# Optimization experiments

Measured on AMD Instinct MI355X. Metric: run time of the kernel, lower is better.

The kernel has to match this reference:

```python
import jax, jax.numpy as jnp
import numpy as np

B, N, NPOINT = 8, 2048, 1024
K = 32
C_IN, C_OUT = 128, 256
PLANES = C_IN // 2   # bottleneck_ratio = 2
MID = PLANES // 2
CURVE_NUM, CURVE_LEN = 100, 5
RADIUS = 0.2
EPS = 1e-5


def bn(x, g, b):
    # training-mode batchnorm over all axes except channel axis 1
    axes = tuple(i for i in range(x.ndim) if i != 1)
    m = jnp.mean(x, axes, keepdims=True)
    v = jnp.var(x, axes, keepdims=True)
    shp = [1] * x.ndim
    shp[1] = -1
    return (x - m) * jax.lax.rsqrt(v + EPS) * g.reshape(shp) + b.reshape(shp)


def conv1d(w, x):  # 1x1 conv, w [O,I], x [B,I,n]
    return jnp.einsum('oi,bin->bon', w, x)


def conv2d(w, x):  # 1x1 conv, w [O,I], x [B,I,n,k]
    return jnp.einsum('oi,bink->bonk', w, x)


def lrelu(x):
    return jax.nn.leaky_relu(x, 0.2)


def gather_points(pts, idx):
    # pts [B,n,C], idx [B,...] int -> [B,...,C]
    b = pts.shape[0]
    out = jnp.take_along_axis(pts, idx.reshape(b, -1)[:, :, None], axis=1)
    return out.reshape(idx.shape + (pts.shape[-1],))


def fps(xyz, npoint):
    # deterministic FPS (torch code zeroes the random start -> index 0)
    bsz, n, _ = xyz.shape
    bidx = jnp.arange(bsz)

    def body(carry, _):
        dist, far = carry
        c = xyz[bidx, far]  # [B,3]
        d = jnp.sum((xyz - c[:, None, :]) ** 2, axis=-1)
        dist = jnp.minimum(dist, d)
        return (dist, jnp.argmax(dist, axis=-1).astype(jnp.int32)), far

    init = (jnp.full((bsz, n), 1e10, xyz.dtype), jnp.zeros((bsz,), jnp.int32))
    _, cents = jax.lax.scan(body, init, None, length=npoint)
    return jnp.transpose(cents)  # [B,npoint]


def knn_idx(pts, k):
    # pts [B,3,n] -> [B,n,k+1] nearest neighbors (self included)
    inner = jnp.einsum('bcn,bcm->bnm', pts, pts)
    xx = jnp.sum(pts * pts, axis=1)
    neg = 2.0 * inner - xx[:, :, None] - xx[:, None, :]
    return jax.lax.top_k(neg, k + 1)[1]


def ball_query(radius, nsample, xyz, new_xyz):
    n = xyz.shape[1]
    sqr = (jnp.sum(new_xyz ** 2, -1)[:, :, None] + jnp.sum(xyz ** 2, -1)[:, None, :]
           - 2.0 * jnp.einsum('bsc,bnc->bsn', new_xyz, xyz))
    gidx = jnp.where(sqr > radius ** 2, n,
                     jnp.arange(n, dtype=jnp.int32)[None, None, :])
    gidx = jnp.sort(gidx, axis=-1)[:, :, :nsample]
    return jnp.where(gidx == n, gidx[:, :, :1], gidx)


def st_gumbel_softmax(logits):
    # straight-through softmax (no gumbel noise, T=1), one-hot over last dim
    y = jax.nn.softmax(logits, axis=-1)
    hard = jax.nn.one_hot(jnp.argmax(y, axis=-1), y.shape[-1], dtype=y.dtype)
    return y + jax.lax.stop_gradient(hard - y)


def walk(x, adj, start, aw, ag, ab, mw, mg, mb):
    # x [B,c,n] attended feats, adj [B,n,K] neighbor idx, start [B,cn]
    xt = jnp.transpose(x, (0, 2, 1))  # [B,n,c]
    cur = start
    pre = jnp.transpose(gather_points(xt, cur), (0, 2, 1))[..., None]  # [B,c,cn,1]
    cur_f = cur_cos = pre_cos = None
    curves = []
    for step in range(CURVE_LEN):
        if step > 0:
            cat = jnp.concatenate([cur_f[..., 0], pre[..., 0]], axis=1)  # [B,2c,cn]
            att = jax.nn.softmax(bn(conv1d(mw, cat), mg, mb), axis=1)    # [B,2,cn]
            att = jnp.transpose(att, (0, 2, 1))[:, None]                 # [B,1,cn,2]
            pre = jnp.sum(jnp.concatenate([cur_f, pre], axis=-1) * att,
                          axis=-1, keepdims=True)
            pre_cos = jnp.transpose(pre[..., 0], (0, 2, 1))              # [B,cn,c]
        pick_idx = jnp.take_along_axis(adj, cur[:, :, None], axis=1)     # [B,cn,K]
        pv = gather_points(xt, pick_idx)                                 # [B,cn,K,c]
        pvt = jnp.transpose(pv, (0, 3, 1, 2))                            # [B,c,cn,K]
        agent_in = jnp.concatenate([pvt, jnp.broadcast_to(pre, pvt.shape)], axis=1)
        logits = bn(conv2d(aw, agent_in), ag, ab)                        # [B,1,cn,K]
        if step > 0:
            a = jax.lax.stop_gradient(cur_cos - pre_cos)                 # [B,cn,c]
            nb = jax.lax.stop_gradient(pv - cur_cos[:, :, None, :])      # [B,cn,K,c]
            dot = jnp.einsum('bnc,bnkc->bnk', a, nb)
            den = jnp.maximum(jnp.linalg.norm(a, axis=-1)[:, :, None]
                              * jnp.linalg.norm(nb, axis=-1), 1e-8)
            d = jnp.clip(1.0 + dot / den, 0.0, 1.0)
            logits = logits * d[:, None]
        w = st_gumbel_softmax(logits)                                    # [B,1,cn,K]
        cur_f = jnp.sum(pvt * w, axis=-1, keepdims=True)                 # [B,c,cn,1]
        cur_cos = jnp.transpose(cur_f[..., 0], (0, 2, 1))
        cur = jnp.argmax(w[:, 0], axis=-1).astype(jnp.int32)
        curves.append(cur_f)
    return jnp.concatenate(curves, axis=-1)  # [B,c,cn,CL]


def curve_agg(x, curves, la, wa, wb, wc, wn, wl, wd, dg, db):
    att = conv2d(la, curves)                                             # [B,1,cn,cl]
    inter = jnp.sum(curves * jax.nn.softmax(att, axis=-1), axis=-1)      # [B,c,cn]
    intra = jnp.sum(curves * jax.nn.softmax(att, axis=-2), axis=-2)      # [B,c,cl]
    inter = conv1d(wa, inter)
    intra = conv1d(wb, intra)
    xl = jnp.transpose(conv1d(wc, x), (0, 2, 1))                         # [B,n,mid]
    x_inter = jax.nn.softmax(jnp.einsum('bnm,bmk->bnk', xl, inter), axis=-1)
    x_intra = jax.nn.softmax(jnp.einsum('bnm,bml->bnl', xl, intra), axis=-1)
    inter_n = jnp.transpose(conv1d(wn, inter), (0, 2, 1))                # [B,cn,mid]
    intra_l = jnp.transpose(conv1d(wl, intra), (0, 2, 1))                # [B,cl,mid]
    cf = jnp.concatenate([jnp.einsum('bnk,bkm->bnm', x_inter, inter_n),
                          jnp.einsum('bnl,blm->bnm', x_intra, intra_l)], axis=-1)
    return lrelu(x + bn(conv1d(wd, jnp.transpose(cf, (0, 2, 1))), dg, db))


def lpfa(x, xyz, idx, xw, xg, xb, w1, g1, b1, w2, g2, b2):
    # x [B,c,n], xyz [B,n,3], idx [B,n,K]
    nb_xyz = gather_points(xyz, idx)                                     # [B,n,K,3]
    pts = xyz[:, :, None, :]
    pf = jnp.concatenate([jnp.broadcast_to(pts, nb_xyz.shape), nb_xyz, nb_xyz - pts],
                         axis=-1)                                        # [B,n,K,9]
    pf = jnp.transpose(pf, (0, 3, 1, 2))                                 # [B,9,n,K]
    xt = jnp.transpose(x, (0, 2, 1))
    f = gather_points(xt, idx) - xt[:, :, None, :]                       # [B,n,K,c]
    f = jnp.transpose(f, (0, 3, 1, 2))                                   # [B,c,n,K]
    f = lrelu(f + bn(conv2d(xw, pf), xg, xb))
    f = lrelu(bn(conv2d(w1, f), g1, b1))
    f = lrelu(bn(conv2d(w2, f), g2, b2))
    return jnp.mean(f, axis=-1)                                          # [B,c,n]


def cic_forward(xyz, x, conv1_w, conv1_g, conv1_b, conv2_w, conv2_g, conv2_b,
                sc_w, sc_g, sc_b, cg_att_w, wk_agent_w, wk_agent_g, wk_agent_b,
                wk_mom_w, wk_mom_g, wk_mom_b, ca_la_w, ca_a_w, ca_b_w, ca_c_w,
                ca_n_w, ca_l_w, ca_d_w, ca_d_g, ca_d_b, lp_x2f_w, lp_x2f_g,
                lp_x2f_b, lp_m1_w, lp_m1_g, lp_m1_b, lp_m2_w, lp_m2_g, lp_m2_b):
    xyz_t = jnp.transpose(xyz, (0, 2, 1))                                # [B,N,3]
    # MaskedMaxPool: FPS -> ball query -> grouped max
    new_xyz = gather_points(xyz_t, fps(xyz_t, NPOINT))                   # [B,np,3]
    gidx = ball_query(RADIUS, K, xyz_t, new_xyz)                         # [B,np,K]
    grouped = gather_points(jnp.transpose(x, (0, 2, 1)), gidx)           # [B,np,K,C]
    x = jnp.transpose(jnp.max(grouped, axis=2), (0, 2, 1))               # [B,C_IN,np]
    xyz_d = jnp.transpose(new_xyz, (0, 2, 1))                            # [B,3,np]
    shortcut = x
    h = lrelu(bn(conv1d(conv1_w, x), conv1_g, conv1_b))                  # [B,P,np]
    idx = knn_idx(xyz_d, K)                                              # [B,np,K+1]
    # CurveGrouping: attention-weighted start point selection + walk
    x_att = jax.nn.sigmoid(conv1d(cg_att_w, h))                          # [B,1,np]
    start = jax.lax.top_k(x_att[:, 0, :], CURVE_NUM)[1].astype(jnp.int32)
    curves = walk(h * x_att, idx[:, :, 1:], start,
                  wk_agent_w, wk_agent_g, wk_agent_b,
                  wk_mom_w, wk_mom_g, wk_mom_b)
    h = curve_agg(h, curves, ca_la_w, ca_a_w, ca_b_w, ca_c_w, ca_n_w, ca_l_w,
                  ca_d_w, ca_d_g, ca_d_b)
    h = lpfa(h, new_xyz, idx[:, :, :K], lp_x2f_w, lp_x2f_g, lp_x2f_b,
             lp_m1_w, lp_m1_g, lp_m1_b, lp_m2_w, lp_m2_g, lp_m2_b)
    out = bn(conv1d(conv2_w, h), conv2_g, conv2_b)
    sc = bn(conv1d(sc_w, shortcut), sc_g, sc_b)
    return xyz_d, lrelu(out + sc)


def setup_inputs() -> dict:
    key = jax.random.key(0)
    ks = iter(jax.random.split(key, 64))

    def w(shape):
        return jax.random.normal(next(ks), shape, jnp.float32) / np.float32(np.sqrt(shape[-1]))

    P, M = PLANES, MID
    return dict(
        xyz=jax.random.uniform(next(ks), (B, 3, N), jnp.float32),
        x=jax.random.normal(next(ks), (B, C_IN, N), jnp.float32),
        conv1_w=w((P, C_IN)), conv1_g=jnp.ones(P), conv1_b=jnp.zeros(P),
        conv2_w=w((C_OUT, P)), conv2_g=jnp.ones(C_OUT), conv2_b=jnp.zeros(C_OUT),
        sc_w=w((C_OUT, C_IN)), sc_g=jnp.ones(C_OUT), sc_b=jnp.zeros(C_OUT),
        cg_att_w=w((1, P)),
        wk_agent_w=w((1, 2 * P)), wk_agent_g=jnp.ones(1), wk_agent_b=jnp.zeros(1),
        wk_mom_w=w((2, 2 * P)), wk_mom_g=jnp.ones(2), wk_mom_b=jnp.zeros(2),
        ca_la_w=w((1, P)),
        ca_a_w=w((M, P)), ca_b_w=w((M, P)), ca_c_w=w((M, P)),
        ca_n_w=w((M, M)), ca_l_w=w((M, M)),
        ca_d_w=w((P, 2 * M)), ca_d_g=jnp.ones(P), ca_d_b=jnp.zeros(P),
        lp_x2f_w=w((P, 9)), lp_x2f_g=jnp.ones(P), lp_x2f_b=jnp.zeros(P),
        lp_m1_w=w((P, P)), lp_m1_g=jnp.ones(P), lp_m1_b=jnp.zeros(P),
        lp_m2_w=w((P, P)), lp_m2_g=jnp.ones(P), lp_m2_b=jnp.zeros(P),
    )


def reference(xyz, x, conv1_w, conv1_g, conv1_b, conv2_w, conv2_g, conv2_b,
              sc_w, sc_g, sc_b, cg_att_w, wk_agent_w, wk_agent_g, wk_agent_b,
              wk_mom_w, wk_mom_g, wk_mom_b, ca_la_w, ca_a_w, ca_b_w, ca_c_w,
              ca_n_w, ca_l_w, ca_d_w, ca_d_g, ca_d_b, lp_x2f_w, lp_x2f_g,
              lp_x2f_b, lp_m1_w, lp_m1_g, lp_m1_b, lp_m2_w, lp_m2_g, lp_m2_b):
    return cic_forward(xyz, x, conv1_w, conv1_g, conv1_b, conv2_w, conv2_g,
                       conv2_b, sc_w, sc_g, sc_b, cg_att_w, wk_agent_w,
                       wk_agent_g, wk_agent_b, wk_mom_w, wk_mom_g, wk_mom_b,
                       ca_la_w, ca_a_w, ca_b_w, ca_c_w, ca_n_w, ca_l_w, ca_d_w,
                       ca_d_g, ca_d_b, lp_x2f_w, lp_x2f_g, lp_x2f_b, lp_m1_w,
                       lp_m1_g, lp_m1_b, lp_m2_w, lp_m2_g, lp_m2_b)
```

## Files before the change

kernel.cpp:

```cpp
#include <hip/hip_runtime.h>
#include <math.h>

namespace {

constexpr int BB = 8;
constexpr int NN = 2048;
constexpr int NP = 1024;
constexpr int KS = 32;
constexpr int CI = 128;
constexpr int CO = 256;
constexpr int PL = 64;
constexpr int MD = 32;
constexpr int CN = 100;
constexpr int CLn = 5;
constexpr float R2v = 0.04f;
constexpr float EPSF = 1e-5f;

#define DEV static __device__ __forceinline__

DEV float lrelu(float x){ return x >= 0.0f ? x : 0.2f * x; }

DEV float wsum64(float v){
#pragma unroll
  for (int m = 32; m; m >>= 1) v += __shfl_xor(v, m, 64);
  return v;
}

DEV unsigned long long dpp_wavemax_u64(unsigned long long v){
  unsigned hi = (unsigned)(v >> 32), lo = (unsigned)v;
#define DSTEP(ctrl) { \
    unsigned nhi = (unsigned)__builtin_amdgcn_update_dpp((int)hi, (int)hi, ctrl, 0xf, 0xf, false); \
    unsigned nlo = (unsigned)__builtin_amdgcn_update_dpp((int)lo, (int)lo, ctrl, 0xf, 0xf, false); \
    bool gt = (nhi > hi) || (nhi == hi && nlo > lo); \
    hi = gt ? nhi : hi; lo = gt ? nlo : lo; }
  DSTEP(0x111)
  DSTEP(0x112)
  DSTEP(0x114)
  DSTEP(0x118)
  DSTEP(0x142)
  DSTEP(0x143)
#undef DSTEP
  hi = (unsigned)__builtin_amdgcn_readlane((int)hi, 63);
  lo = (unsigned)__builtin_amdgcn_readlane((int)lo, 63);
  return ((unsigned long long)hi << 32) | lo;
}

DEV int dpp_argmax_idx(float v, int idx){
  unsigned kb = __float_as_uint(v);
  kb = (kb & 0x80000000u) ? ~kb : (kb | 0x80000000u);
  unsigned long long p = ((unsigned long long)kb << 32) | (unsigned)~idx;
  return (int)~(unsigned)dpp_wavemax_u64(p);
}

__global__ __launch_bounds__(256) void k_fps(const float* __restrict__ xyz,
                                             float* __restrict__ nxyz, float* __restrict__ nxx){
  int b = blockIdx.x, t = threadIdx.x, w = t >> 6;
  const float* X = xyz + (size_t)b*3*NN;
  __shared__ unsigned long long sk[2][4];
  __shared__ float4 scd[2][4];
  float px[8], py[8], pz[8], dd[8];
  int base = t*8;
#pragma unroll
  for (int j=0;j<8;++j){
    px[j]=X[base+j]; py[j]=X[NN+base+j]; pz[j]=X[2*NN+base+j];
    dd[j]=1e10f;
  }
  float cx = X[0], cy = X[NN], cz = X[2*NN];
  float ox[4], oy[4], oz[4];
#pragma unroll
  for (int p=0;p<4;++p){
    for (int j=0;j<256;++j){
      if (j == t){ ox[p]=cx; oy[p]=cy; oz[p]=cz; }
#pragma unroll
      for (int q=0;q<8;++q){
        float dx=__fsub_rn(px[q],cx), dy=__fsub_rn(py[q],cy), dz=__fsub_rn(pz[q],cz);
        float dn=__fadd_rn(__fadd_rn(__fmul_rn(dx,dx),__fmul_rn(dy,dy)),__fmul_rn(dz,dz));
        dd[q] = fminf(dd[q], dn);
      }
      float v = dd[0]; int li = 0;
#pragma unroll
      for (int q=1;q<8;++q) if (dd[q] > v){ v = dd[q]; li = q; }
      float wx = px[0], wy = py[0], wz = pz[0];
#pragma unroll
      for (int q=1;q<8;++q) if (li == q){ wx=px[q]; wy=py[q]; wz=pz[q]; }
      unsigned long long key = ((unsigned long long)__float_as_uint(v) << 32) | (unsigned)~(base+li);
      unsigned long long wm = dpp_wavemax_u64(key);
      if (key == wm){ sk[j&1][w] = wm; scd[j&1][w] = make_float4(wx,wy,wz,0.f); }
      __syncthreads();
      unsigned long long k0=sk[j&1][0], k1=sk[j&1][1], k2=sk[j&1][2], k3=sk[j&1][3];
      float4 c0=scd[j&1][0], c1=scd[j&1][1], c2=scd[j&1][2], c3=scd[j&1][3];
      if (k1 > k0){ k0=k1; c0=c1; }
      if (k2 > k0){ k0=k2; c0=c2; }
      if (k3 > k0){ k0=k3; c0=c3; }
      cx = c0.x; cy = c0.y; cz = c0.z;
    }
  }
#pragma unroll
  for (int p=0;p<4;++p){
    size_t o = (size_t)(b*NP + (p<<8) + t);
    nxyz[o*3+0]=ox[p]; nxyz[o*3+1]=oy[p]; nxyz[o*3+2]=oz[p];
    nxx[o] = __fadd_rn(__fadd_rn(__fmul_rn(ox[p],ox[p]),__fmul_rn(oy[p],oy[p])),__fmul_rn(oz[p],oz[p]));
  }
}

__global__ __launch_bounds__(256) void k_ball(const float* __restrict__ xyz,
                      const float* __restrict__ nxyz, const float* __restrict__ nxx,
                      int* __restrict__ gidx){
  __shared__ int lists[4][KS];
  int t = threadIdx.x, w = t>>6, lane = t&63;
  int s = blockIdx.x*4 + w;
  int b = s >> 10;
  const float* X = xyz + (size_t)b*3*NN;
  float cx = nxyz[s*3], cy = nxyz[s*3+1], cz = nxyz[s*3+2];
  float cn = nxx[s];
  unsigned long long lmask = (lane == 63) ? 0x7fffffffffffffffull : ((1ull<<lane)-1ull);
  int cnt = 0;
  for (int ch = 0; ch < NN/64; ++ch){
    int n = ch*64 + lane;
    float px = X[n], py = X[NN+n], pz = X[2*NN+n];
    float nrm = __fadd_rn(__fadd_rn(__fmul_rn(px,px),__fmul_rn(py,py)),__fmul_rn(pz,pz));
    float dot = __fadd_rn(__fadd_rn(__fmul_rn(cx,px),__fmul_rn(cy,py)),__fmul_rn(cz,pz));
    float sqr = __fsub_rn(__fadd_rn(cn, nrm), __fmul_rn(2.0f, dot));
    bool inr = !(sqr > R2v);
    unsigned long long m = __ballot(inr);
    if (inr){
      int slot = cnt + __popcll(m & lmask);
      if (slot < KS) lists[w][slot] = n;
    }
    cnt += __popcll(m);
    if (cnt >= KS) break;
  }
  int take = cnt < KS ? cnt : KS;
  if (lane < KS){
    gidx[(size_t)s*KS + lane] = lists[w][lane < take ? lane : 0];
  }
}

__global__ __launch_bounds__(256) void k_transpose(const float* __restrict__ x, float* __restrict__ xt){
  __shared__ float tile[32][33];
  int blk = blockIdx.x;
  int b = blk >> 8;
  int r = blk & 255;
  int nt = r >> 2, ct = r & 3;
  int tx = threadIdx.x & 31, ty = threadIdx.x >> 5;
  const float* Xb = x + (size_t)b*CI*NN;
#pragma unroll
  for (int q=0;q<4;++q){
    int row = ty + q*8;
    tile[row][tx] = Xb[(size_t)(ct*32+row)*NN + nt*32 + tx];
  }
  __syncthreads();
  float* Tb = xt + (size_t)b*NN*CI;
#pragma unroll
  for (int q=0;q<4;++q){
    int row = ty + q*8;
    Tb[(size_t)(nt*32+row)*CI + ct*32 + tx] = tile[tx][row];
  }
}

__global__ __launch_bounds__(128) void k_groupmax(const float* __restrict__ xt, const int* __restrict__ gidx,
                          float* __restrict__ xnew){
  int s = blockIdx.x;
  int b = s >> 10;
  int c = threadIdx.x;
  const int* gi = gidx + (size_t)s*KS;
  float m = -INFINITY;
#pragma unroll 4
  for (int k=0;k<KS;++k){
    int idx = gi[k];
    m = fmaxf(m, xt[((size_t)b*NN + idx)*CI + c]);
  }
  xnew[(size_t)s*CI + c] = m;
}

__global__ __launch_bounds__(256) void k_conv1(const float* __restrict__ xnew, const float* __restrict__ w,
                       float* __restrict__ hraw, float* __restrict__ part){
  __shared__ float wl[PL*129];
  __shared__ float xr[4][CI];
  __shared__ float ssm[4][PL], sq[4][PL];
  int t = threadIdx.x, wid = t>>6, lane = t&63;
  for (int u=t; u<PL*CI; u+=256){ int c=u>>7, i=u&127; wl[c*129+i] = w[u]; }
  int pt = blockIdx.x*4 + wid;
  xr[wid][lane]      = xnew[(size_t)pt*CI + lane];
  xr[wid][lane+64]   = xnew[(size_t)pt*CI + lane + 64];
  __syncthreads();
  float acc = 0.f;
  for (int i=0;i<CI;++i) acc = __fadd_rn(acc, __fmul_rn(wl[lane*129+i], xr[wid][i]));
  hraw[(size_t)pt*PL + lane] = acc;
  ssm[wid][lane] = acc; sq[wid][lane] = acc*acc;
  __syncthreads();
  if (t < PL){
    float s=0,q=0;
#pragma unroll
    for (int k=0;k<4;++k){ s+=ssm[k][t]; q+=sq[k][t]; }
    part[((size_t)blockIdx.x*PL + t)*2]   = s;
    part[((size_t)blockIdx.x*PL + t)*2+1] = q;
  }
}

__global__ __launch_bounds__(256) void k_red(const float* __restrict__ part, float* __restrict__ mv,
                     int nblk, int C2){
  int slot = blockIdx.x;
  __shared__ float red[256];
  float s = 0;
  for (int i = threadIdx.x; i < nblk; i += 256) s += part[(size_t)i*C2 + slot];
  red[threadIdx.x] = s; __syncthreads();
  for (int off=128; off; off>>=1){ if (threadIdx.x < off) red[threadIdx.x] += red[threadIdx.x+off]; __syncthreads(); }
  if (threadIdx.x==0) mv[slot] = red[0];
}

__global__ __launch_bounds__(256) void k_n1(const float* __restrict__ hraw, const float* __restrict__ mv,
                    const float* __restrict__ g, const float* __restrict__ bb_, const float* __restrict__ attw,
                    float* __restrict__ h, float* __restrict__ attv, float* __restrict__ wxt){
  int t=threadIdx.x, wid=t>>6, lane=t&63;
  int pt = blockIdx.x*4 + wid;
  float x = hraw[(size_t)pt*PL + lane];
  float m = mv[2*lane] * (1.0f/8192.0f);
  float var = fmaxf(mv[2*lane+1]*(1.0f/8192.0f) - m*m, 0.f);
  float rs = 1.0f/sqrtf(var + EPSF);
  float hv = lrelu(__fadd_rn(__fmul_rn(__fmul_rn(__fsub_rn(x,m),rs), g[lane]), bb_[lane]));
  h[(size_t)pt*PL + lane] = hv;
  float dotv = wsum64(__fmul_rn(hv, attw[lane]));
  float att = 1.0f/(1.0f + expf(-dotv));
  if (lane==0) attv[pt] = att;
  wxt[(size_t)pt*PL + lane] = __fmul_rn(hv, att);
}

__global__ __launch_bounds__(256) void k_knn(const float* __restrict__ nxyz, const float* __restrict__ nxx,
                     int* __restrict__ knnI){
  int t=threadIdx.x, wid=t>>6, lane=t&63;
  int gn = blockIdx.x*4 + wid;
  int b = gn >> 10;
  float cx = nxyz[(size_t)gn*3], cy=nxyz[(size_t)gn*3+1], cz=nxyz[(size_t)gn*3+2];
  float xn = nxx[gn];
  float vals[16];
#pragma unroll
  for (int q=0;q<16;++q){
    int mm = b*NP + q*64 + lane;
    float px=nxyz[(size_t)mm*3], py=nxyz[(size_t)mm*3+1], pz=nxyz[(size_t)mm*3+2];
    float dot = __fadd_rn(__fadd_rn(__fmul_rn(cx,px),__fmul_rn(cy,py)),__fmul_rn(cz,pz));
    vals[q] = __fsub_rn(__fsub_rn(__fmul_rn(2.0f,dot), xn), nxx[mm]);
  }
  int* out = knnI + (size_t)gn*33;
  for (int j=0;j<33;++j){
    float bv = -INFINITY; int bq = 0;
#pragma unroll
    for (int q=0;q<16;++q) if (vals[q] > bv){ bv = vals[q]; bq = q; }
    int vi = dpp_argmax_idx(bv, (bq<<6) | lane);
    if (lane == 0) out[j] = vi;
    if ((vi & 63) == lane){
      int wq = vi>>6;
#pragma unroll
      for (int q=0;q<16;++q) if (q==wq) vals[q] = -INFINITY;
    }
  }
}

__global__ __launch_bounds__(64) void k_start(const float* __restrict__ attv, int* __restrict__ startb){
  int b = blockIdx.x, lane = threadIdx.x;
  float vals[16];
#pragma unroll
  for (int q=0;q<16;++q) vals[q] = attv[b*NP + q*64 + lane];
  for (int j=0;j<CN;++j){
    float bv=-INFINITY; int bq=0;
#pragma unroll
    for (int q=0;q<16;++q) if (vals[q] > bv){ bv=vals[q]; bq=q; }
    int vi = dpp_argmax_idx(bv, (bq<<6) | lane);
    if (lane==0) startb[b*CN + j] = vi;
    if ((vi&63)==lane){
      int wq=vi>>6;
#pragma unroll
      for(int q=0;q<16;++q) if(q==wq) vals[q]=-INFINITY;
    }
  }
}

__global__ __launch_bounds__(256) void k_w0(const float* __restrict__ wxt, const int* __restrict__ startb,
                    float* __restrict__ pre, int* __restrict__ curidx){
  int t=threadIdx.x, wid=t>>6, lane=t&63;
  int gc = blockIdx.x*4+wid;
  int b = gc/CN;
  int si = startb[gc];
  pre[(size_t)gc*PL + lane] = wxt[((size_t)b*NP+si)*PL + lane];
  if (lane==0) curidx[gc] = si;
}

__global__ __launch_bounds__(256) void k_wmom(const float* __restrict__ curf, float* __restrict__ pre,
                      const float* __restrict__ mw, const float* __restrict__ mg, const float* __restrict__ mb_){
  __shared__ float m0a[BB*CN], m1a[BB*CN];
  __shared__ float red[256][4];
  __shared__ float bc[4];
  int t = threadIdx.x;
  float s0=0,q0=0,s1=0,q1=0;
  for (int u=t; u<BB*CN; u+=256){
    const float4* cf4 = reinterpret_cast<const float4*>(curf + (size_t)u*PL);
    const float4* pr4 = reinterpret_cast<const float4*>(pre + (size_t)u*PL);
    float a0=0, a1=0;
#pragma unroll
    for (int i4=0;i4<16;++i4){
      float4 c = cf4[i4];
      a0=__fadd_rn(a0,__fmul_rn(mw[i4*4+0],c.x));     a0=__fadd_rn(a0,__fmul_rn(mw[i4*4+1],c.y));
      a0=__fadd_rn(a0,__fmul_rn(mw[i4*4+2],c.z));     a0=__fadd_rn(a0,__fmul_rn(mw[i4*4+3],c.w));
      a1=__fadd_rn(a1,__fmul_rn(mw[128+i4*4+0],c.x)); a1=__fadd_rn(a1,__fmul_rn(mw[128+i4*4+1],c.y));
      a1=__fadd_rn(a1,__fmul_rn(mw[128+i4*4+2],c.z)); a1=__fadd_rn(a1,__fmul_rn(mw[128+i4*4+3],c.w));
    }
#pragma unroll
    for (int i4=0;i4<16;++i4){
      float4 p = pr4[i4];
      a0=__fadd_rn(a0,__fmul_rn(mw[64+i4*4+0],p.x));  a0=__fadd_rn(a0,__fmul_rn(mw[64+i4*4+1],p.y));
      a0=__fadd_rn(a0,__fmul_rn(mw[64+i4*4+2],p.z));  a0=__fadd_rn(a0,__fmul_rn(mw[64+i4*4+3],p.w));
      a1=__fadd_rn(a1,__fmul_rn(mw[192+i4*4+0],p.x)); a1=__fadd_rn(a1,__fmul_rn(mw[192+i4*4+1],p.y));
      a1=__fadd_rn(a1,__fmul_rn(mw[192+i4*4+2],p.z)); a1=__fadd_rn(a1,__fmul_rn(mw[192+i4*4+3],p.w));
    }
    m0a[u]=a0; m1a[u]=a1;
    s0+=a0; q0+=a0*a0; s1+=a1; q1+=a1*a1;
  }
  red[t][0]=s0; red[t][1]=q0; red[t][2]=s1; red[t][3]=q1;
  __syncthreads();
  for (int off=128; off; off>>=1){
    if (t<off){ red[t][0]+=red[t+off][0]; red[t][1]+=red[t+off][1]; red[t][2]+=red[t+off][2]; red[t][3]+=red[t+off][3]; }
    __syncthreads();
  }
  if (t==0){
    float me0 = red[0][0]/800.0f, va0 = fmaxf(red[0][1]/800.0f - me0*me0, 0.f);
    float me1 = red[0][2]/800.0f, va1 = fmaxf(red[0][3]/800.0f - me1*me1, 0.f);
    bc[0]=me0; bc[1]=1.0f/sqrtf(va0+EPSF); bc[2]=me1; bc[3]=1.0f/sqrtf(va1+EPSF);
  }
  __syncthreads();
  float me0=bc[0], rs0=bc[1], me1=bc[2], rs1=bc[3];
  float g0=mg[0], g1=mg[1], b0=mb_[0], b1=mb_[1];
  for (int u=t; u<BB*CN; u+=256){
    float z0 = __fadd_rn(__fmul_rn(__fmul_rn(__fsub_rn(m0a[u],me0),rs0),g0), b0);
    float z1 = __fadd_rn(__fmul_rn(__fmul_rn(__fsub_rn(m1a[u],me1),rs1),g1), b1);
    float mx = fmaxf(z0,z1);
    float e0 = expf(z0-mx), e1 = expf(z1-mx);
    float se = e0+e1;
    float a0 = e0/se, a1 = e1/se;
    float4* pr4 = reinterpret_cast<float4*>(pre + (size_t)u*PL);
    const float4* cf4 = reinterpret_cast<const float4*>(curf + (size_t)u*PL);
#pragma unroll
    for (int c4=0;c4<16;++c4){
      float4 cv = cf4[c4], pv_ = pr4[c4], r;
      r.x = __fadd_rn(__fmul_rn(cv.x,a0), __fmul_rn(pv_.x,a1));
      r.y = __fadd_rn(__fmul_rn(cv.y,a0), __fmul_rn(pv_.y,a1));
      r.z = __fadd_rn(__fmul_rn(cv.z,a0), __fmul_rn(pv_.z,a1));
      r.w = __fadd_rn(__fmul_rn(cv.w,a0), __fmul_rn(pv_.w,a1));
      pr4[c4] = r;
    }
  }
}

__global__ __launch_bounds__(256) void k_w2(const float* __restrict__ wxt, const float* __restrict__ pre,
                    const int* __restrict__ knnI, const int* __restrict__ curidx,
                    const float* __restrict__ aw,
                    float* __restrict__ pv, float* __restrict__ logitb, float* __restrict__ part){
  __shared__ float red[256];
  __shared__ int nbrs[8][32];
  int t=threadIdx.x;
  int gcw = t>>5, k = t & 31;
  int gc0 = blockIdx.x*8;
  int gc = gc0 + gcw;
  int b = gc/CN;
  int cc = curidx[gc];
  int nbr = knnI[((size_t)b*NP + cc)*33 + 1 + k];
  nbrs[gcw][k] = nbr;
  __syncthreads();
  int lane = t & 63, w = t >> 6;
#pragma unroll 4
  for (int r = w; r < 256; r += 4){
    int rg = r >> 5, rk = r & 31;
    int rb = (gc0 + rg)/CN;
    pv[((size_t)(gc0+rg)*KS + rk)*PL + lane] = wxt[((size_t)rb*NP + nbrs[rg][rk])*PL + lane];
  }
  __syncthreads();
  const float* row = pv + ((size_t)gc*KS + k)*PL;
  const float* pr = pre + (size_t)gc*PL;
  float acc=0;
  for (int i=0;i<PL;++i){ acc=__fadd_rn(acc,__fmul_rn(aw[i],row[i])); }
  for (int i=0;i<PL;++i){ acc=__fadd_rn(acc,__fmul_rn(aw[PL+i],pr[i])); }
  logitb[(size_t)gc*KS + k] = acc;
  red[t]=acc; __syncthreads();
  for (int off=128; off; off>>=1){ if(t<off) red[t]+=red[t+off]; __syncthreads(); }
  float tot = red[0];
  __syncthreads();
  red[t]=acc*acc; __syncthreads();
  for (int off=128; off; off>>=1){ if(t<off) red[t]+=red[t+off]; __syncthreads(); }
  if (t==0){ part[blockIdx.x*2]=tot; part[blockIdx.x*2+1]=red[0]; }
}

__global__ __launch_bounds__(64) void k_w3(const float* __restrict__ pv, const float* __restrict__ logitb,
                   const float* __restrict__ part, float* __restrict__ curf,
                   const float* __restrict__ pre, float* __restrict__ curves, int* __restrict__ curidx,
                   const float* __restrict__ ag, const float* __restrict__ ab_, int step){
  __shared__ int ks_;
  __shared__ float wv_;
  int gc = blockIdx.x;
  int lane = threadIdx.x;
  float s=0,q=0;
  for (int u=lane; u<100; u+=64){ s+=part[2*u]; q+=part[2*u+1]; }
  s = wsum64(s); q = wsum64(q);
  float me = s/25600.0f;
  float va = fmaxf(q/25600.0f - me*me, 0.f);
  float rs = 1.0f/sqrtf(va+EPSF);
  float g0 = ag[0], b0 = ab_[0];
// ... 232 lines not shown
  __shared__ int   nbl[4][KS];
  __shared__ __align__(16) float fbuf[4][PL*36];
  __shared__ float ssm[4][PL], sq[4][PL];
  int t=threadIdx.x, wid=t>>6, lane=t&63;
  int pt = blockIdx.x*4+wid;
  int b = pt >> 10;
  if (lane < KS){
    int nb = knnI[(size_t)pt*33 + lane];
    nbl[wid][lane] = nb;
    float cx=nxyz[(size_t)pt*3], cy=nxyz[(size_t)pt*3+1], cz=nxyz[(size_t)pt*3+2];
    size_t nbg = (size_t)b*NP + nb;
    float nx=nxyz[nbg*3], ny=nxyz[nbg*3+1], nz=nxyz[nbg*3+2];
    float* pf = &pfb[wid][lane*10];
    pf[0]=cx; pf[1]=cy; pf[2]=cz; pf[3]=nx; pf[4]=ny; pf[5]=nz;
    pf[6]=__fsub_rn(nx,cx); pf[7]=__fsub_rn(ny,cy); pf[8]=__fsub_rn(nz,cz);
  }
  __syncthreads();
  float xwr[9];
#pragma unroll
  for (int i=0;i<9;++i) xwr[i] = xw[lane*9+i];
  float c1v[KS];
#pragma unroll
  for (int j=0;j<KS;++j){
    float a=0;
#pragma unroll
    for (int i=0;i<9;++i) a = fmaf(xwr[i], pfb[wid][j*10+i], a);
    c1v[j]=a;
  }
  if (STAGE == 1){
    float s=0,qq=0;
#pragma unroll
    for (int j=0;j<KS;++j){ s+=c1v[j]; qq+=c1v[j]*c1v[j]; }
    ssm[wid][lane]=s; sq[wid][lane]=qq;
    __syncthreads();
    if (t<PL){
      float s2=0,q2=0;
#pragma unroll
      for(int k2=0;k2<4;++k2){s2+=ssm[k2][t];q2+=sq[k2][t];}
      part[((size_t)blockIdx.x*PL+t)*2]=s2; part[((size_t)blockIdx.x*PL+t)*2+1]=q2;
    }
    return;
  }
  constexpr float CT = 1.0f/262144.0f;
  float m1 = mv1[2*lane]*CT; float va1=fmaxf(mv1[2*lane+1]*CT-m1*m1,0.f); float rs1=1.0f/sqrtf(va1+EPSF);
  float hc = h2[(size_t)pt*PL + lane];
  float g1v=g1[lane], b1v=b1[lane];
#pragma unroll
  for (int j=0;j<KS;++j){
    float fd = __fsub_rn(h2[((size_t)b*NP + nbl[wid][j])*PL + lane], hc);
    float bn1 = __fadd_rn(__fmul_rn(__fmul_rn(__fsub_rn(c1v[j],m1),rs1),g1v),b1v);
    fbuf[wid][lane*36+j] = lrelu(__fadd_rn(fd, bn1));
  }
  __syncthreads();
  float wr[PL];
#pragma unroll
  for (int i=0;i<PL;++i) wr[i] = w1[lane*PL+i];
  float acc[KS];
#pragma unroll
  for (int j=0;j<KS;++j) acc[j]=0;
#pragma unroll
  for (int cp=0;cp<PL;++cp){
    const float4* rp = reinterpret_cast<const float4*>(&fbuf[wid][cp*36]);
    float wv = wr[cp];
#pragma unroll
    for (int j4=0;j4<8;++j4){
      float4 f = rp[j4];
      acc[j4*4+0] = fmaf(wv, f.x, acc[j4*4+0]);
      acc[j4*4+1] = fmaf(wv, f.y, acc[j4*4+1]);
      acc[j4*4+2] = fmaf(wv, f.z, acc[j4*4+2]);
      acc[j4*4+3] = fmaf(wv, f.w, acc[j4*4+3]);
    }
  }
  if (STAGE == 2){
    float s=0,qq=0;
#pragma unroll
    for (int j=0;j<KS;++j){ s+=acc[j]; qq+=acc[j]*acc[j]; }
    ssm[wid][lane]=s; sq[wid][lane]=qq;
    __syncthreads();
    if (t<PL){
      float s2=0,q2=0;
#pragma unroll
      for(int k2=0;k2<4;++k2){s2+=ssm[k2][t];q2+=sq[k2][t];}
      part[((size_t)blockIdx.x*PL+t)*2]=s2; part[((size_t)blockIdx.x*PL+t)*2+1]=q2;
    }
    return;
  }
  float m2 = mv2[2*lane]*CT; float va2=fmaxf(mv2[2*lane+1]*CT-m2*m2,0.f); float rs2=1.0f/sqrtf(va2+EPSF);
  float g2v=g2[lane], b2v=b2[lane];
  __syncthreads();
#pragma unroll
  for (int j=0;j<KS;++j){
    float f2 = lrelu(__fadd_rn(__fmul_rn(__fmul_rn(__fsub_rn(acc[j],m2),rs2),g2v),b2v));
    fbuf[wid][lane*36+j] = f2;
  }
  __syncthreads();
#pragma unroll
  for (int i=0;i<PL;++i) wr[i] = w2[lane*PL+i];
#pragma unroll
  for (int j=0;j<KS;++j) acc[j]=0;
#pragma unroll
  for (int cp=0;cp<PL;++cp){
    const float4* rp = reinterpret_cast<const float4*>(&fbuf[wid][cp*36]);
    float wv = wr[cp];
#pragma unroll
    for (int j4=0;j4<8;++j4){
      float4 f = rp[j4];
      acc[j4*4+0] = fmaf(wv, f.x, acc[j4*4+0]);
      acc[j4*4+1] = fmaf(wv, f.y, acc[j4*4+1]);
      acc[j4*4+2] = fmaf(wv, f.z, acc[j4*4+2]);
      acc[j4*4+3] = fmaf(wv, f.w, acc[j4*4+3]);
    }
  }
  if (STAGE == 3){
    float s=0,qq=0;
#pragma unroll
    for (int j=0;j<KS;++j){ s+=acc[j]; qq+=acc[j]*acc[j]; }
    ssm[wid][lane]=s; sq[wid][lane]=qq;
    __syncthreads();
    if (t<PL){
      float s2=0,q2=0;
#pragma unroll
      for(int k2=0;k2<4;++k2){s2+=ssm[k2][t];q2+=sq[k2][t];}
      part[((size_t)blockIdx.x*PL+t)*2]=s2; part[((size_t)blockIdx.x*PL+t)*2+1]=q2;
    }
    return;
  }
  float m3 = mv3[2*lane]*CT; float va3=fmaxf(mv3[2*lane+1]*CT-m3*m3,0.f); float rs3=1.0f/sqrtf(va3+EPSF);
  float g3v=g3[lane], b3v=b3[lane];
  float sum=0;
#pragma unroll
  for (int j=0;j<KS;++j){
    float f3 = lrelu(__fadd_rn(__fmul_rn(__fmul_rn(__fsub_rn(acc[j],m3),rs3),g3v),b3v));
    sum = __fadd_rn(sum, f3);
  }
  lpout[(size_t)pt*PL + lane] = __fmul_rn(sum, (1.0f/32.0f));
}

__global__ __launch_bounds__(256) void k_fc1(const float* __restrict__ lpout, const float* __restrict__ w,
                     float* __restrict__ y2raw, float* __restrict__ part){
  __shared__ float wl[128*65];
  __shared__ float xr[4][PL];
  __shared__ float ssm[4][128], sq[4][128];
  int t=threadIdx.x, wid=t>>6, lane=t&63;
  int pg = blockIdx.x >> 1;
  int half = blockIdx.x & 1;
  int pt = pg*4 + wid;
  for (int u=t; u<128*PL; u+=256){ int c=u>>6, i=u&63; wl[c*65+i] = w[(size_t)half*128*PL + u]; }
  xr[wid][lane] = lpout[(size_t)pt*PL + lane];
  __syncthreads();
  float a0=0, a1=0;
  for (int i=0;i<PL;++i){
    float xv = xr[wid][i];
    a0 = fmaf(wl[lane*65+i], xv, a0);
    a1 = fmaf(wl[(lane+64)*65+i], xv, a1);
  }
  y2raw[(size_t)pt*CO + half*128 + lane]      = a0;
  y2raw[(size_t)pt*CO + half*128 + 64 + lane] = a1;
  ssm[wid][lane]=a0; ssm[wid][64+lane]=a1; sq[wid][lane]=a0*a0; sq[wid][64+lane]=a1*a1;
  __syncthreads();
  if (t < 128){
    float s=0,qq=0;
#pragma unroll
    for(int k2=0;k2<4;++k2){ s+=ssm[k2][t]; qq+=sq[k2][t]; }
    part[((size_t)pg*CO + half*128 + t)*2]   = s;
    part[((size_t)pg*CO + half*128 + t)*2+1] = qq;
  }
}

__global__ __launch_bounds__(256) void k_fc2(const float* __restrict__ xnew, const float* __restrict__ w,
                     float* __restrict__ scraw, float* __restrict__ part){
  __shared__ float wl[64*129];
  __shared__ float xr[4][CI];
  __shared__ float ssm[4][64], sq[4][64];
  int t=threadIdx.x, wid=t>>6, lane=t&63;
  int pg = blockIdx.x >> 2;
  int qr = blockIdx.x & 3;
  int pt = pg*4 + wid;
  for (int u=t; u<64*CI; u+=256){ int c=u>>7, i=u&127; wl[c*129+i] = w[(size_t)qr*64*CI + u]; }
  xr[wid][lane]    = xnew[(size_t)pt*CI+lane];
  xr[wid][lane+64] = xnew[(size_t)pt*CI+lane+64];
  __syncthreads();
  float a=0;
  for (int i=0;i<CI;++i) a = fmaf(wl[lane*129+i], xr[wid][i], a);
  scraw[(size_t)pt*CO + qr*64 + lane] = a;
  ssm[wid][lane]=a; sq[wid][lane]=a*a;
  __syncthreads();
  if (t<64){
    float s=0,qq=0;
#pragma unroll
    for(int k2=0;k2<4;++k2){ s+=ssm[k2][t]; qq+=sq[k2][t]; }
    part[((size_t)pg*CO + qr*64 + t)*2]   = s;
    part[((size_t)pg*CO + qr*64 + t)*2+1] = qq;
  }
}

__global__ __launch_bounds__(256) void k_fc3(const float* __restrict__ y2raw, const float* __restrict__ scraw,
                     const float* __restrict__ mvfc, const float* __restrict__ mvsc,
                     const float* __restrict__ g2, const float* __restrict__ b2,
                     const float* __restrict__ gs, const float* __restrict__ bs,
                     float* __restrict__ outp){
  int u = blockIdx.x*256+threadIdx.x;
  int p = u & 1023;
  int c = (u >> 10) & 255;
  int b = u >> 18;
  float mo = mvfc[2*c]*(1.0f/8192.0f); float vo=fmaxf(mvfc[2*c+1]*(1.0f/8192.0f)-mo*mo,0.f); float ro=1.0f/sqrtf(vo+EPSF);
  float ms = mvsc[2*c]*(1.0f/8192.0f); float vs=fmaxf(mvsc[2*c+1]*(1.0f/8192.0f)-ms*ms,0.f); float rs=1.0f/sqrtf(vs+EPSF);
  float y = y2raw[((size_t)b*NP+p)*CO + c];
  float s = scraw[((size_t)b*NP+p)*CO + c];
  float v1 = __fadd_rn(__fmul_rn(__fmul_rn(__fsub_rn(y,mo),ro),g2[c]), b2[c]);
  float v2 = __fadd_rn(__fmul_rn(__fmul_rn(__fsub_rn(s,ms),rs),gs[c]), bs[c]);
  outp[u] = lrelu(__fadd_rn(v1,v2));
}

__global__ void k_xyzd(const float* __restrict__ nxyz, float* __restrict__ outp){
  int u = blockIdx.x*256+threadIdx.x; if (u >= BB*3*NP) return;
  int s = u & 1023;
  int c = (u>>10)%3;
  int b = u/(3*NP);
  outp[u] = nxyz[((size_t)b*NP+s)*3 + c];
}

}

extern "C" void kernel_launch(void* const* d_in, const int* in_sizes, int n_in,
                              void* d_out, int out_size, void* d_ws, size_t ws_size,
                              hipStream_t stream){
  const float* xyz  = (const float*)d_in[0];
  const float* xin  = (const float*)d_in[1];
  const float* c1w  = (const float*)d_in[2];
  const float* c1g  = (const float*)d_in[3];
  const float* c1b  = (const float*)d_in[4];
  const float* c2w  = (const float*)d_in[5];
  const float* c2g  = (const float*)d_in[6];
  const float* c2b  = (const float*)d_in[7];
  const float* scw  = (const float*)d_in[8];
  const float* scg  = (const float*)d_in[9];
  const float* scb  = (const float*)d_in[10];
  const float* attw = (const float*)d_in[11];
  const float* aw   = (const float*)d_in[12];
  const float* ag   = (const float*)d_in[13];
  const float* abv  = (const float*)d_in[14];
  const float* mw   = (const float*)d_in[15];
  const float* mg   = (const float*)d_in[16];
  const float* mb_  = (const float*)d_in[17];
  const float* law  = (const float*)d_in[18];
  const float* waw  = (const float*)d_in[19];
  const float* wbw  = (const float*)d_in[20];
  const float* wcw  = (const float*)d_in[21];
  const float* wnw  = (const float*)d_in[22];
  const float* wlw  = (const float*)d_in[23];
  const float* wdw  = (const float*)d_in[24];
  const float* dg   = (const float*)d_in[25];
  const float* db   = (const float*)d_in[26];
  const float* xfw  = (const float*)d_in[27];
  const float* xfg  = (const float*)d_in[28];
  const float* xfb  = (const float*)d_in[29];
  const float* m1w  = (const float*)d_in[30];
  const float* m1g  = (const float*)d_in[31];
  const float* m1b  = (const float*)d_in[32];
  const float* m2w  = (const float*)d_in[33];
  const float* m2g  = (const float*)d_in[34];
  const float* m2b  = (const float*)d_in[35];
  float* outp = (float*)d_out;

  char* base = (char*)d_ws;
  size_t off = 0;
  auto alloc = [&](size_t nbytes)->void*{ void* p = base + off; off = (off + nbytes + 255) & ~(size_t)255; return p; };
  float* nxyz   = (float*)alloc(sizeof(float)*BB*NP*3);
  float* nxx    = (float*)alloc(sizeof(float)*BB*NP);
  int*   gidx   = (int*)  alloc(sizeof(int)*BB*NP*KS);
  float* xt     = (float*)alloc(sizeof(float)*(size_t)BB*NN*CI);
  float* xnew   = (float*)alloc(sizeof(float)*(size_t)BB*NP*CI);
  float* hraw   = (float*)alloc(sizeof(float)*(size_t)BB*NP*PL);
  float* hbuf   = (float*)alloc(sizeof(float)*(size_t)BB*NP*PL);
  float* attv   = (float*)alloc(sizeof(float)*BB*NP);
  float* wxt    = (float*)alloc(sizeof(float)*(size_t)BB*NP*PL);
  int*   knnI   = (int*)  alloc(sizeof(int)*BB*NP*33);
  int*   startb = (int*)  alloc(sizeof(int)*BB*CN);
  float* pre    = (float*)alloc(sizeof(float)*BB*CN*PL);
  float* curf   = (float*)alloc(sizeof(float)*BB*CN*PL);
  int*   curidx = (int*)  alloc(sizeof(int)*BB*CN);
  float* pv     = (float*)alloc(sizeof(float)*(size_t)BB*CN*KS*PL);
  float* logitb = (float*)alloc(sizeof(float)*BB*CN*KS);
  float* curves = (float*)alloc(sizeof(float)*BB*CN*CLn*PL);
  float* inter1 = (float*)alloc(sizeof(float)*BB*CN*MD);
  float* intern = (float*)alloc(sizeof(float)*BB*CN*MD);
  float* intra1 = (float*)alloc(sizeof(float)*BB*CLn*MD);
  float* intral = (float*)alloc(sizeof(float)*BB*CLn*MD);
  float* yraw   = (float*)alloc(sizeof(float)*(size_t)BB*NP*PL);
  float* h2     = (float*)alloc(sizeof(float)*(size_t)BB*NP*PL);
  float* lpout  = (float*)alloc(sizeof(float)*(size_t)BB*NP*PL);
  float* y2raw  = (float*)alloc(sizeof(float)*(size_t)BB*NP*CO);
  float* scraw  = (float*)alloc(sizeof(float)*(size_t)BB*NP*CO);
  float* part   = (float*)alloc(sizeof(float)*(size_t)2048*CO*2);
  float* mvA    = (float*)alloc(sizeof(float)*2048);
  float* mvC1 = mvA;
  float* mvWD = mvA + 128;
  float* mvL1 = mvA + 256;
  float* mvL2 = mvA + 384;
  float* mvL3 = mvA + 512;
  float* mvFC = mvA + 640;
  float* mvSC = mvA + 1152;

  k_fps<<<BB, 256, 0, stream>>>(xyz, nxyz, nxx);
  k_ball<<<(BB*NP)/4, 256, 0, stream>>>(xyz, nxyz, nxx, gidx);
  k_transpose<<<BB*256, 256, 0, stream>>>(xin, xt);
  k_groupmax<<<BB*NP, 128, 0, stream>>>(xt, gidx, xnew);
  k_conv1<<<(BB*NP)/4, 256, 0, stream>>>(xnew, c1w, hraw, part);
  k_red<<<128, 256, 0, stream>>>(part, mvC1, 2048, 128);
  k_n1<<<(BB*NP)/4, 256, 0, stream>>>(hraw, mvC1, c1g, c1b, attw, hbuf, attv, wxt);
  k_knn<<<(BB*NP)/4, 256, 0, stream>>>(nxyz, nxx, knnI);
  k_start<<<BB, 64, 0, stream>>>(attv, startb);
  k_w0<<<(BB*CN)/4, 256, 0, stream>>>(wxt, startb, pre, curidx);
  for (int step = 0; step < CLn; ++step){
    if (step > 0) k_wmom<<<1, 256, 0, stream>>>(curf, pre, mw, mg, mb_);
    k_w2<<<(BB*CN)/8, 256, 0, stream>>>(wxt, pre, knnI, curidx, aw, pv, logitb, part);
    k_w3<<<BB*CN, 64, 0, stream>>>(pv, logitb, part, curf, pre, curves, curidx, ag, abv, step);
  }
  k_cagg<<<BB, 256, 0, stream>>>(curves, law, waw, wbw, wnw, wlw, inter1, intern, intra1, intral);
  k_ca5<<<(BB*NP)/4, 256, 0, stream>>>(hbuf, inter1, intern, intra1, intral, wcw, wdw, yraw, part);
  k_red<<<128, 256, 0, stream>>>(part, mvWD, 2048, 128);
  k_ca7<<<(BB*NP*PL)/256, 256, 0, stream>>>(hbuf, yraw, mvWD, dg, db, h2);
  k_lp<1><<<(BB*NP)/4, 256, 0, stream>>>(nxyz, knnI, h2, xfw, m1w, m2w, mvL1, mvL2, mvL3, xfg, xfb, m1g, m1b, m2g, m2b, part, lpout);
  k_red<<<128, 256, 0, stream>>>(part, mvL1, 2048, 128);
  k_lp<2><<<(BB*NP)/4, 256, 0, stream>>>(nxyz, knnI, h2, xfw, m1w, m2w, mvL1, mvL2, mvL3, xfg, xfb, m1g, m1b, m2g, m2b, part, lpout);
  k_red<<<128, 256, 0, stream>>>(part, mvL2, 2048, 128);
  k_lp<3><<<(BB*NP)/4, 256, 0, stream>>>(nxyz, knnI, h2, xfw, m1w, m2w, mvL1, mvL2, mvL3, xfg, xfb, m1g, m1b, m2g, m2b, part, lpout);
  k_red<<<128, 256, 0, stream>>>(part, mvL3, 2048, 128);
  k_lp<4><<<(BB*NP)/4, 256, 0, stream>>>(nxyz, knnI, h2, xfw, m1w, m2w, mvL1, mvL2, mvL3, xfg, xfb, m1g, m1b, m2g, m2b, part, lpout);
  k_fc1<<<((BB*NP)/4)*2, 256, 0, stream>>>(lpout, c2w, y2raw, part);
  k_red<<<512, 256, 0, stream>>>(part, mvFC, 2048, 512);
  k_fc2<<<((BB*NP)/4)*4, 256, 0, stream>>>(xnew, scw, scraw, part);
  k_red<<<512, 256, 0, stream>>>(part, mvSC, 2048, 512);
  k_fc3<<<(BB*CO*NP)/256, 256, 0, stream>>>(y2raw, scraw, mvFC, mvSC, c2g, c2b, scg, scb, outp + BB*3*NP);
  k_xyzd<<<(BB*3*NP + 255)/256, 256, 0, stream>>>(nxyz, outp);
}
```

Baseline: 1.757 ms.

## Run FPS in a single wavefront per batch to remove block barriers

Farthest point sampling now uses one 64-lane wave per batch, with 32 points per lane held in registers, instead of a 256-thread block. Each iteration no longer needs a cross-wave __syncthreads and shared-memory key exchange. The argmax is split into two 32-bit DPP reductions: a max over the distances, then a min over the indices that hold that max. The winning coordinates come from a copy of all points kept in LDS. This trades the barrier cost for four times more serial arithmetic per lane and higher register use on a kernel that only launches eight blocks.

```diff
diff --git a/kernel.cpp b/kernel.cpp
--- a/kernel.cpp
+++ b/kernel.cpp
@@ -52,54 +52,65 @@
   return (int)~(unsigned)dpp_wavemax_u64(p);
 }
 
-__global__ __launch_bounds__(256) void k_fps(const float* __restrict__ xyz,
-                                             float* __restrict__ nxyz, float* __restrict__ nxx){
-  int b = blockIdx.x, t = threadIdx.x, w = t >> 6;
+DEV unsigned dpp_wavemax_u32(unsigned v){
+#define ST(ctrl) { unsigned o = (unsigned)__builtin_amdgcn_update_dpp((int)v,(int)v,ctrl,0xf,0xf,false); v = o>v?o:v; }
+  ST(0x111) ST(0x112) ST(0x114) ST(0x118) ST(0x142) ST(0x143)
+#undef ST
+  return (unsigned)__builtin_amdgcn_readlane((int)v,63);
+}
+DEV unsigned dpp_wavemin_u32(unsigned v){
+#define ST(ctrl) { unsigned o = (unsigned)__builtin_amdgcn_update_dpp((int)v,(int)v,ctrl,0xf,0xf,false); v = o<v?o:v; }
+  ST(0x111) ST(0x112) ST(0x114) ST(0x118) ST(0x142) ST(0x143)
+#undef ST
+  return (unsigned)__builtin_amdgcn_readlane((int)v,63);
+}
+
+__global__ __launch_bounds__(64) void k_fps(const float* __restrict__ xyz,
+                                            float* __restrict__ nxyz, float* __restrict__ nxx){
+  int b = blockIdx.x, lane = threadIdx.x;
   const float* X = xyz + (size_t)b*3*NN;
-  __shared__ unsigned long long sk[2][4];
-  __shared__ float4 scd[2][4];
-  float px[8], py[8], pz[8], dd[8];
-  int base = t*8;
-#pragma unroll
-  for (int j=0;j<8;++j){
-    px[j]=X[base+j]; py[j]=X[NN+base+j]; pz[j]=X[2*NN+base+j];
-    dd[j]=1e10f;
-  }
+  __shared__ float4 cpk[NN];
+  float px[32], py[32], pz[32], dd[32];
+#pragma unroll
+  for (int q=0;q<32;++q){
+    int n = q*64 + lane;
+    px[q]=X[n]; py[q]=X[NN+n]; pz[q]=X[2*NN+n];
+    dd[q]=1e10f;
+    cpk[n] = make_float4(px[q], py[q], pz[q], 0.f);
+  }
+  __syncthreads();
   float cx = X[0], cy = X[NN], cz = X[2*NN];
-  float ox[4], oy[4], oz[4];
-#pragma unroll
-  for (int p=0;p<4;++p){
-    for (int j=0;j<256;++j){
-      if (j == t){ ox[p]=cx; oy[p]=cy; oz[p]=cz; }
-#pragma unroll
-      for (int q=0;q<8;++q){
-        float dx=__fsub_rn(px[q],cx), dy=__fsub_rn(py[q],cy), dz=__fsub_rn(pz[q],cz);
-        float dn=__fadd_rn(__fadd_rn(__fmul_rn(dx,dx),__fmul_rn(dy,dy)),__fmul_rn(dz,dz));
-        dd[q] = fminf(dd[q], dn);
-      }
-      float v = dd[0]; int li = 0;
-#pragma unroll
-      for (int q=1;q<8;++q) if (dd[q] > v){ v = dd[q]; li = q; }
-      float wx = px[0], wy = py[0], wz = pz[0];
-#pragma unroll
-      for (int q=1;q<8;++q) if (li == q){ wx=px[q]; wy=py[q]; wz=pz[q]; }
-      unsigned long long key = ((unsigned long long)__float_as_uint(v) << 32) | (unsigned)~(base+li);
-      unsigned long long wm = dpp_wavemax_u64(key);
-      if (key == wm){ sk[j&1][w] = wm; scd[j&1][w] = make_float4(wx,wy,wz,0.f); }
-      __syncthreads();
-      unsigned long long k0=sk[j&1][0], k1=sk[j&1][1], k2=sk[j&1][2], k3=sk[j&1][3];
-      float4 c0=scd[j&1][0], c1=scd[j&1][1], c2=scd[j&1][2], c3=scd[j&1][3];
-      if (k1 > k0){ k0=k1; c0=c1; }
-      if (k2 > k0){ k0=k2; c0=c2; }
-      if (k3 > k0){ k0=k3; c0=c3; }
-      cx = c0.x; cy = c0.y; cz = c0.z;
-    }
-  }
-#pragma unroll
-  for (int p=0;p<4;++p){
-    size_t o = (size_t)(b*NP + (p<<8) + t);
-    nxyz[o*3+0]=ox[p]; nxyz[o*3+1]=oy[p]; nxyz[o*3+2]=oz[p];
-    nxx[o] = __fadd_rn(__fadd_rn(__fmul_rn(ox[p],ox[p]),__fmul_rn(oy[p],oy[p])),__fmul_rn(oz[p],oz[p]));
+  for (int it = 0; it < NP; ++it){
+    if (lane == 0){
+      nxyz[(size_t)(b*NP+it)*3+0] = cx;
+      nxyz[(size_t)(b*NP+it)*3+1] = cy;
+      nxyz[(size_t)(b*NP+it)*3+2] = cz;
+      nxx[b*NP+it] = __fadd_rn(__fadd_rn(__fmul_rn(cx,cx),__fmul_rn(cy,cy)),__fmul_rn(cz,cz));
+    }
+#pragma unroll
+    for (int q=0;q<32;++q){
+      float dx=__fsub_rn(px[q],cx), dy=__fsub_rn(py[q],cy), dz=__fsub_rn(pz[q],cz);
+      float dn=__fadd_rn(__fadd_rn(__fmul_rn(dx,dx),__fmul_rn(dy,dy)),__fmul_rn(dz,dz));
+      dd[q] = fminf(dd[q], dn);
+    }
+    unsigned m[32];
+#pragma unroll
+    for (int q=0;q<32;++q) m[q] = __float_as_uint(dd[q]);
+#pragma unroll
+    for (int s=16;s;s>>=1)
+#pragma unroll
+      for (int i=0;i<16;++i) if (i<s) m[i] = m[i] > m[i+s] ? m[i] : m[i+s];
+    unsigned gmax = dpp_wavemax_u32(m[0]);
+    unsigned idx[32];
+#pragma unroll
+    for (int q=0;q<32;++q) idx[q] = (__float_as_uint(dd[q])==gmax) ? (unsigned)(q*64+lane) : 0xffffffffu;
+#pragma unroll
+    for (int s=16;s;s>>=1)
+#pragma unroll
+      for (int i=0;i<16;++i) if (i<s) idx[i] = idx[i] < idx[i+s] ? idx[i] : idx[i+s];
+    unsigned gbest = dpp_wavemin_u32(idx[0]);
+    float4 c = cpk[gbest];
+    cx = c.x; cy = c.y; cz = c.z;
   }
 }
 
@@ -938,7 +949,7 @@
   float* mvFC = mvA + 640;
   float* mvSC = mvA + 1152;
 
-  k_fps<<<BB, 256, 0, stream>>>(xyz, nxyz, nxx);
+  k_fps<<<BB, 64, 0, stream>>>(xyz, nxyz, nxx);
   k_ball<<<(BB*NP)/4, 256, 0, stream>>>(xyz, nxyz, nxx, gidx);
   k_transpose<<<BB*256, 256, 0, stream>>>(xin, xt);
   k_groupmax<<<BB*NP, 128, 0, stream>>>(xt, gidx, xnew);
```

Result: slower. 2.074 ms (+18.0%).
